# Performance work log

Hardware: AMD Instinct MI355X
Metric: run time of the kernel (lower is better)

## Reference

```python
import jax, jax.numpy as jnp
import numpy as np

B, N = 8, 32768
S1, S2, K = 512, 128, 32


def _knn_idx(refs, queries, k):
    # refs: (B,S,D), queries: (B,Q,D) -> (B,Q,k) indices of k nearest refs
    d = (jnp.sum(queries * queries, -1)[:, :, None]
         - 2.0 * jnp.einsum('bqd,bsd->bqs', queries, refs)
         + jnp.sum(refs * refs, -1)[:, None, :])
    _, idx = jax.lax.top_k(-d, k)
    return idx


def _gather(feats, idx):
    # feats: (B,S,C), idx: (B,Q,k) -> (B,Q,k,C)
    return jax.vmap(lambda f, i: f[i])(feats, idx)


def _mlp(x, w1, b1, w2, b2):
    # pointwise (1x1 conv) MLP: Linear -> ReLU -> Linear
    return jnp.maximum(x @ w1 + b1, 0.0) @ w2 + b2


def _set_abstraction(coords, feats, samp_idx, k, w1, b1, w2, b2):
    centers = coords[:, samp_idx]                 # (B,S,D)
    nidx = _knn_idx(coords, centers, k)           # (B,S,k)
    groups = _gather(feats, nidx)                 # (B,S,k,C)
    h = _mlp(groups, w1, b1, w2, b2)              # (B,S,k,C_out)
    return jnp.max(h, axis=2), centers


def _feature_prop(coords_q, feats_q, coords_s, feats_s, w1, b1, w2, b2):
    nidx = _knn_idx(coords_s, coords_q, 3)        # (B,Q,3)
    interp = jnp.mean(_gather(feats_s, nidx), axis=2)  # 3-NN average (sum/3)
    return _mlp(jnp.concatenate([feats_q, interp], -1), w1, b1, w2, b2)


def setup_inputs():
    key = jax.random.key(0)
    ks = jax.random.split(key, 12)

    def w(k, shape):
        return jax.random.normal(k, shape, jnp.float32) * 0.05

    z = lambda c: jnp.zeros((c,), jnp.float32)
    return {
        'x': jax.random.normal(ks[0], (B, N, 3), jnp.float32),
        'sa1_w1': w(ks[1], (3, 64)),   'sa1_b1': z(64),
        'sa1_w2': w(ks[2], (64, 64)),  'sa1_b2': z(64),
        'sa2_w1': w(ks[3], (64, 128)), 'sa2_b1': z(128),
        'sa2_w2': w(ks[4], (128, 128)),'sa2_b2': z(128),
        'fp1_w1': w(ks[5], (192, 64)), 'fp1_b1': z(64),
        'fp1_w2': w(ks[6], (64, 64)),  'fp1_b2': z(64),
        'fp2_w1': w(ks[7], (67, 32)),  'fp2_b1': z(32),
        'fp2_w2': w(ks[8], (32, 32)),  'fp2_b2': z(32),
        'fc_w': w(ks[9], (32, 2)),     'fc_b': z(2),
    }


def reference(x, sa1_w1, sa1_b1, sa1_w2, sa1_b2,
              sa2_w1, sa2_b1, sa2_w2, sa2_b2,
              fp1_w1, fp1_b1, fp1_w2, fp1_b2,
              fp2_w1, fp2_b1, fp2_w2, fp2_b2,
              fc_w, fc_b):
    rng = np.random.default_rng(0)
    samp1 = jnp.asarray(rng.permutation(N)[:S1])   # torch.randperm analog (static)
    samp2 = jnp.asarray(rng.permutation(S1)[:S2])

    f1, s1 = _set_abstraction(x, x, samp1, K, sa1_w1, sa1_b1, sa1_w2, sa1_b2)
    f2, s2 = _set_abstraction(s1, f1, samp2, K, sa2_w1, sa2_b1, sa2_w2, sa2_b2)
    g1 = _feature_prop(s1, f1, s2, f2, fp1_w1, fp1_b1, fp1_w2, fp1_b2)   # (B,512,64)
    g2 = _feature_prop(x, x, s1, g1, fp2_w1, fp2_b1, fp2_w2, fp2_b2)     # (B,N,32)
    logits = g2 @ fc_w + fc_b                                            # (B,N,2)
    return jax.nn.log_softmax(logits, axis=-1)
```

## Files before the change

### kernel.cpp

```cpp
#include <hip/hip_runtime.h>
#include <stdint.h>

#define B_ 8
#define N_ 32768
#define S1_ 512
#define S2_ 128

#define OFF_XR4   ((size_t)0)
#define OFF_C1    ((size_t)4194304)
#define OFF_C1R4  ((size_t)4243456)
#define OFF_C2    ((size_t)4308992)
#define OFF_NIDX1 ((size_t)4321280)
#define OFF_F1    ((size_t)4845568)
#define OFF_NIDX2 ((size_t)5369856)
#define OFF_F2    ((size_t)5500928)
#define OFF_G1    ((size_t)6025216)

struct Samps { int s1[S1_]; int s2[S2_]; };

typedef unsigned __int128 u128;
struct RngState { u128 state, inc; bool has32; uint32_t saved; };

static uint64_t rng_next64(RngState* r) {
  const u128 MULT = ((u128)0x2360ed051fc65da4ULL << 64) | 0x4385df649fccf645ULL;
  r->state = r->state * MULT + r->inc;
  uint64_t hi = (uint64_t)(r->state >> 64), lo = (uint64_t)r->state;
  uint64_t xs = hi ^ lo;
  unsigned rot = (unsigned)(r->state >> 122);
  return (xs >> rot) | (xs << ((64u - rot) & 63u));
}
static uint32_t rng_next32(RngState* r) {
  if (r->has32) { r->has32 = false; return r->saved; }
  uint64_t v = rng_next64(r);
  r->has32 = true; r->saved = (uint32_t)(v >> 32);
  return (uint32_t)v;
}
static uint32_t rng_interval(RngState* r, uint32_t mx) {
  if (mx == 0) return 0;
  uint32_t mask = mx;
  mask |= mask >> 1; mask |= mask >> 2; mask |= mask >> 4;
  mask |= mask >> 8; mask |= mask >> 16;
  uint32_t v;
  while ((v = (rng_next32(r) & mask)) > mx) {}
  return v;
}
static void compute_samples(int* s1, int* s2) {
  uint32_t pool[4];
  uint32_t hc = 0x43b0d7e5u;
  auto hmix = [&hc](uint32_t v) -> uint32_t {
    v ^= hc; hc *= 0x931e8875u; v *= hc; v ^= v >> 16; return v;
  };
  auto mixf = [](uint32_t x, uint32_t y) -> uint32_t {
    uint32_t rr = (x * 0xca01f9ddu) ^ (y * 0x4973f715u);
    rr ^= rr >> 16; return rr;
  };
  pool[0] = hmix(0u); pool[1] = hmix(0u); pool[2] = hmix(0u); pool[3] = hmix(0u);
  for (int s = 0; s < 4; ++s)
    for (int d = 0; d < 4; ++d)
      if (s != d) pool[d] = mixf(pool[d], hmix(pool[s]));
  uint32_t hc2 = 0x8b51f9ddu;
  uint32_t w32[8];
  for (int i = 0; i < 8; ++i) {
    uint32_t dv = pool[i & 3];
    dv ^= hc2; hc2 *= 0x58f38dedu; dv *= hc2; dv ^= dv >> 16;
    w32[i] = dv;
  }
  uint64_t w64[4];
  for (int i = 0; i < 4; ++i) w64[i] = (uint64_t)w32[2*i] | ((uint64_t)w32[2*i+1] << 32);
  const u128 MULT = ((u128)0x2360ed051fc65da4ULL << 64) | 0x4385df649fccf645ULL;
  u128 initstate = ((u128)w64[0] << 64) | w64[1];
  u128 initseq   = ((u128)w64[2] << 64) | w64[3];
  RngState r; r.has32 = false; r.saved = 0;
  r.inc = (initseq << 1) | 1;
  r.state = 0;
  r.state = r.state * MULT + r.inc;
  r.state += initstate;
  r.state = r.state * MULT + r.inc;
  static int perm1[N_];
  for (int i = 0; i < N_; ++i) perm1[i] = i;
  for (int i = N_ - 1; i > 0; --i) {
    uint32_t j = rng_interval(&r, (uint32_t)i);
    int t = perm1[i]; perm1[i] = perm1[j]; perm1[j] = t;
  }
  for (int i = 0; i < S1_; ++i) s1[i] = perm1[i];
  int perm2[S1_];
  for (int i = 0; i < S1_; ++i) perm2[i] = i;
  for (int i = S1_ - 1; i > 0; --i) {
    uint32_t j = rng_interval(&r, (uint32_t)i);
    int t = perm2[i]; perm2[i] = perm2[j]; perm2[j] = t;
  }
  for (int i = 0; i < S2_; ++i) s2[i] = perm2[i];
}


__global__ void k_prep(const float* __restrict__ x, float4* __restrict__ xr4) {
  int t = blockIdx.x * blockDim.x + threadIdx.x;
  float a = x[3*t], b = x[3*t+1], c = x[3*t+2];
  xr4[t] = make_float4(a, b, c, a*a + b*b + c*c);
}

__global__ void k_centers(const float* __restrict__ x, Samps sm,
                          float* __restrict__ c1, float4* __restrict__ c1r4,
                          float* __restrict__ c2) {
  int t = blockIdx.x * blockDim.x + threadIdx.x;
  if (t < B_*S1_) {
    int b = t >> 9, c = t & (S1_-1);
    int sidx = sm.s1[c];
    const float* src = x + ((size_t)b*N_ + sidx)*3;
    float a = src[0], bb = src[1], cc = src[2];
    c1[(size_t)t*3+0] = a; c1[(size_t)t*3+1] = bb; c1[(size_t)t*3+2] = cc;
    c1r4[t] = make_float4(a, bb, cc, a*a + bb*bb + cc*cc);
  } else {
    int u = t - B_*S1_;
    if (u < B_*S2_) {
      int b = u >> 7, c = u & (S2_-1);
      int sidx = sm.s1[sm.s2[c]];
      const float* src = x + ((size_t)b*N_ + sidx)*3;
      c2[(size_t)u*3+0] = src[0]; c2[(size_t)u*3+1] = src[1]; c2[(size_t)u*3+2] = src[2];
    }
  }
}

#define KNN_KEY(RV, UB)                                                     \
  {                                                                         \
    float dot = qx*(RV).x + qy*(RV).y + qz*(RV).z;                          \
    float dd = (qq - 2.0f*dot) + (RV).w;                                    \
    (UB) = __float_as_uint(dd);                                             \
    (UB) ^= ((unsigned int)((int)(UB) >> 31)) | 0x80000000u;                \
  }

#define KNN_INSERT(UB, PBASE)                                               \
  {                                                                         \
    bool cand = ((UB) < T);                                                 \
    while (__any(cand)) {                                                   \
      unsigned long long bal = __ballot(cand);                              \
      int src = (int)__builtin_ctzll(bal);                                  \
      unsigned int ikd = (unsigned int)__shfl((int)(UB), src);              \
      unsigned int iki = (unsigned int)((PBASE) + src);                     \
      int pos = __popcll(__ballot(ld <= ikd));                              \
      unsigned int ud = (unsigned int)__shfl_up((int)ld, 1);                \
      unsigned int ui = (unsigned int)__shfl_up((int)li, 1);                \
      if (lane == pos)      { ld = ikd; li = iki; }                         \
      else if (lane > pos)  { ld = ud;  li = ui;  }                         \
      T = (unsigned int)__shfl((int)ld, 31);                                \
      cand = cand && ((UB) < T) && (lane != src);                           \
    }                                                                       \
  }

__launch_bounds__(256)
__global__ void k_knn(const float4* __restrict__ refs4, const float* __restrict__ qpts,
                      int* __restrict__ out_idx, int nrefs, int qshift) {
  const int tid = threadIdx.x, lane = tid & 63;
  const int q = blockIdx.x * 4 + (tid >> 6);
  const int b = q >> qshift;
  const float4* refs = refs4 + (size_t)b * nrefs;
  float qx = qpts[(size_t)q*3+0], qy = qpts[(size_t)q*3+1], qz = qpts[(size_t)q*3+2];
  float qq = qx*qx + qy*qy + qz*qz;
  unsigned int ld, li, T;
  {
    float4 rv = refs[lane];
    unsigned int ub; KNN_KEY(rv, ub);
    unsigned long long key = ((unsigned long long)ub << 32) | (unsigned int)lane;
    #pragma unroll
    for (int k2 = 2; k2 <= 64; k2 <<= 1) {
      #pragma unroll
      for (int j = k2 >> 1; j >= 1; j >>= 1) {
        unsigned long long o = __shfl_xor(key, j);
        bool keepmin = (((lane & j) == 0) == ((lane & k2) == 0));
        if ((o < key) == keepmin) key = o;
      }
    }
    ld = (unsigned int)(key >> 32);
    li = (unsigned int)key;
    T = (unsigned int)__shfl((int)ld, 31);
  }
  {
    float4 r1 = refs[64 + lane];
    float4 r2 = refs[128 + lane];
    float4 r3 = refs[192 + lane];
    unsigned int u1, u2, u3;
    KNN_KEY(r1, u1); KNN_KEY(r2, u2); KNN_KEY(r3, u3);
    KNN_INSERT(u1, 64);
    KNN_INSERT(u2, 128);
    KNN_INSERT(u3, 192);
  }
  for (int g = 256; g + 255 < nrefs; g += 256) {
    float4 r0 = refs[g + lane];
    float4 r1 = refs[g + 64 + lane];
    float4 r2 = refs[g + 128 + lane];
    float4 r3 = refs[g + 192 + lane];
    unsigned int u0, u1, u2, u3;
    KNN_KEY(r0, u0); KNN_KEY(r1, u1); KNN_KEY(r2, u2); KNN_KEY(r3, u3);
    KNN_INSERT(u0, g);
    KNN_INSERT(u1, g + 64);
    KNN_INSERT(u2, g + 128);
    KNN_INSERT(u3, g + 192);
  }
  if (lane < 32) out_idx[(size_t)q*32 + lane] = (int)li;
}

__launch_bounds__(256)
__global__ void k_sa1mlp(const float* __restrict__ x, const int* __restrict__ nidx1,
                         const float* __restrict__ w1, const float* __restrict__ b1,
                         const float* __restrict__ w2, const float* __restrict__ b2,
                         float* __restrict__ f1) {
  __shared__ __align__(16) float hbuf[4][64];
  const int tid = threadIdx.x, wave = tid >> 6, lane = tid & 63;
  const int q = blockIdx.x * 4 + wave;
  const int b = q >> 9;
  const float* xb = x + (size_t)b * N_ * 3;
  float wc0 = w1[lane], wc1 = w1[64 + lane], wc2 = w1[128 + lane];
  float b1v = b1[lane], b2v = b2[lane];
  float w2c[64];
  #pragma unroll
  for (int h = 0; h < 64; ++h) w2c[h] = w2[h*64 + lane];
  const int* nb = nidx1 + (size_t)q * 32;
  int n0 = nb[0];
  float px = xb[3*n0], py = xb[3*n0+1], pz = xb[3*n0+2];
  float fm = -3.402823466e+38f;
  for (int j = 0; j < 32; ++j) {
    int n2 = nb[(j + 1) & 31];
    float nx = xb[3*n2], ny = xb[3*n2+1], nz = xb[3*n2+2];
    float h1 = fmaf(px, wc0, fmaf(py, wc1, fmaf(pz, wc2, b1v)));
    h1 = fmaxf(h1, 0.0f);
    hbuf[wave][lane] = h1;
    float acc = b2v;
    const float4* hv = (const float4*)(&hbuf[wave][0]);
    #pragma unroll
    for (int h4 = 0; h4 < 16; ++h4) {
      float4 v = hv[h4];
      acc = fmaf(v.x, w2c[4*h4+0], acc);
      acc = fmaf(v.y, w2c[4*h4+1], acc);
      acc = fmaf(v.z, w2c[4*h4+2], acc);
      acc = fmaf(v.w, w2c[4*h4+3], acc);
    }
    fm = fmaxf(fm, acc);
    px = nx; py = ny; pz = nz;
  }
  f1[(size_t)q*64 + lane] = fm;
}

__launch_bounds__(256)
__global__ void k_sa2mlp(const float* __restrict__ f1, const int* __restrict__ nidx2,
                         const float* __restrict__ w1, const float* __restrict__ b1,
                         const float* __restrict__ w2, const float* __restrict__ b2,
                         float* __restrict__ f2) {
  __shared__ __align__(16) float fin[64];
  __shared__ __align__(16) float h1s[128];
  __shared__ float ph[128];
  const int tid = threadIdx.x;
  const int s = tid >> 7, t = tid & 127;
  const int q = blockIdx.x;
  const int b = q >> 7;
  float w1r[32], w2r[64];
  #pragma unroll
  for (int i = 0; i < 32; ++i) w1r[i] = w1[(s*32 + i)*128 + t];
  #pragma unroll
  for (int h = 0; h < 64; ++h) w2r[h] = w2[(s*64 + h)*128 + t];
  float b1v = b1[t], b2v = b2[t];
  const int* nb = nidx2 + (size_t)q * 32;
  float fm = -3.402823466e+38f;
  for (int j = 0; j < 32; ++j) {
    int n = nb[j];
    __syncthreads();
    if (tid < 64) fin[tid] = f1[((size_t)b * S1_ + n)*64 + tid];
    __syncthreads();
    float p1 = 0.0f;
    const float4* fv = (const float4*)(fin + s*32);
    #pragma unroll
    for (int i4 = 0; i4 < 8; ++i4) {
      float4 v = fv[i4];
      p1 = fmaf(v.x, w1r[4*i4+0], p1);
      p1 = fmaf(v.y, w1r[4*i4+1], p1);
      p1 = fmaf(v.z, w1r[4*i4+2], p1);
      p1 = fmaf(v.w, w1r[4*i4+3], p1);
    }
    if (s) ph[t] = p1;
    __syncthreads();
    if (!s) h1s[t] = fmaxf(p1 + ph[t] + b1v, 0.0f);
    __syncthreads();
    float p2 = 0.0f;
    const float4* hv = (const float4*)(h1s + s*64);
    #pragma unroll
    for (int h4 = 0; h4 < 16; ++h4) {
      float4 v = hv[h4];
      p2 = fmaf(v.x, w2r[4*h4+0], p2);
      p2 = fmaf(v.y, w2r[4*h4+1], p2);
      p2 = fmaf(v.z, w2r[4*h4+2], p2);
      p2 = fmaf(v.w, w2r[4*h4+3], p2);
    }
    if (s) ph[t] = p2;
    __syncthreads();
    if (!s) fm = fmaxf(fm, p2 + ph[t] + b2v);
  }
  if (!s) f2[(size_t)q*128 + t] = fm;
}

__launch_bounds__(256)
__global__ void k_fp1(const float* __restrict__ c1, const float* __restrict__ c2,
                      const float* __restrict__ f1, const float* __restrict__ f2,
                      const float* __restrict__ w1, const float* __restrict__ b1,
                      const float* __restrict__ w2, const float* __restrict__ b2,
                      float* __restrict__ g1) {
  __shared__ __align__(16) float sw1[192*64];
  __shared__ __align__(16) float sw2[64*64];
  __shared__ __align__(16) float sinp[4][192];
  __shared__ __align__(16) float sh1[4][64];
  __shared__ __align__(16) float4 srefs4[S2_];
  const int tid = threadIdx.x;
  const int wave = tid >> 6, lane = tid & 63;
  const int q = blockIdx.x * 4 + wave;
  const int b = q >> 9;
  for (int i = tid; i < 192*64; i += 256) sw1[i] = w1[i];
  for (int i = tid; i < 64*64; i += 256) sw2[i] = w2[i];
  if (tid < S2_) {
    const float* rp = c2 + ((size_t)b * S2_ + tid) * 3;
    float rx = rp[0], ry = rp[1], rz = rp[2];
    srefs4[tid] = make_float4(rx, ry, rz, rx*rx + ry*ry + rz*rz);
  }
  __syncthreads();
  float qx = c1[(size_t)q*3+0], qy = c1[(size_t)q*3+1], qz = c1[(size_t)q*3+2];
  float qq = qx*qx + qy*qy + qz*qz;
  unsigned long long ka, kb;
  {
    float4 rv = srefs4[lane];
    float dot = qx*rv.x + qy*rv.y + qz*rv.z;
    float d = (qq - 2.0f*dot) + rv.w;
    unsigned int ub = __float_as_uint(d);
    ub ^= ((unsigned int)((int)ub >> 31)) | 0x80000000u;
    ka = ((unsigned long long)ub << 32) | (unsigned int)lane;
    rv = srefs4[lane + 64];
    dot = qx*rv.x + qy*rv.y + qz*rv.z;
    d = (qq - 2.0f*dot) + rv.w;
    ub = __float_as_uint(d);
    ub ^= ((unsigned int)((int)ub >> 31)) | 0x80000000u;
    kb = ((unsigned long long)ub << 32) | (unsigned int)(lane + 64);
    if (kb < ka) { unsigned long long tt = ka; ka = kb; kb = tt; }
  }
  int nsel[3];
  #pragma unroll
  for (int r = 0; r < 3; ++r) {
    unsigned long long m = ka;
    #pragma unroll
    for (int s = 1; s < 64; s <<= 1) {
      unsigned long long o = __shfl_xor(m, s);
      if (o < m) m = o;
    }
    nsel[r] = (int)(m & 0xffffffffu);
    if (ka == m) { ka = kb; kb = ~0ULL; }
  }
  const float* f2b = f2 + (size_t)b * S2_ * 128;
  sinp[wave][lane] = f1[(size_t)q*64 + lane];
  {
    float a0 = f2b[(size_t)nsel[0]*128 + lane];
    float a1 = f2b[(size_t)nsel[1]*128 + lane];
    float a2 = f2b[(size_t)nsel[2]*128 + lane];
    sinp[wave][64 + lane] = (a0 + a1 + a2) / 3.0f;
    a0 = f2b[(size_t)nsel[0]*128 + 64 + lane];
    a1 = f2b[(size_t)nsel[1]*128 + 64 + lane];
    a2 = f2b[(size_t)nsel[2]*128 + 64 + lane];
    sinp[wave][128 + lane] = (a0 + a1 + a2) / 3.0f;
  }
  __syncthreads();
  float acc = b1[lane];
  const float4* sv = (const float4*)(&sinp[wave][0]);
  #pragma unroll
  for (int i4 = 0; i4 < 48; ++i4) {
    float4 v = sv[i4];
    acc = fmaf(v.x, sw1[(4*i4+0)*64 + lane], acc);
    acc = fmaf(v.y, sw1[(4*i4+1)*64 + lane], acc);
    acc = fmaf(v.z, sw1[(4*i4+2)*64 + lane], acc);
    acc = fmaf(v.w, sw1[(4*i4+3)*64 + lane], acc);
  }
  sh1[wave][lane] = fmaxf(acc, 0.0f);
  __syncthreads();
  float acc2 = b2[lane];
  const float4* hv = (const float4*)(&sh1[wave][0]);
  #pragma unroll
  for (int h4 = 0; h4 < 16; ++h4) {
    float4 v = hv[h4];
    acc2 = fmaf(v.x, sw2[(4*h4+0)*64 + lane], acc2);
    acc2 = fmaf(v.y, sw2[(4*h4+1)*64 + lane], acc2);
    acc2 = fmaf(v.z, sw2[(4*h4+2)*64 + lane], acc2);
    acc2 = fmaf(v.w, sw2[(4*h4+3)*64 + lane], acc2);
  }
  g1[(size_t)q*64 + lane] = acc2;
}

#define FP2_PROC(RV, R)                                                     \
  {                                                                         \
    float dot = qx*(RV).x + qy*(RV).y + qz*(RV).z;                          \
    float dd = (qq - 2.0f*dot) + (RV).w;                                    \
    bool c0 = dd < d0, c1 = dd < d1, c2 = dd < d2;                          \
    i2 = c1 ? i1 : (c2 ? (R) : i2);                                         \
    d2 = c1 ? d1 : fminf(d2, dd);                                           \
    i1 = c0 ? i0 : (c1 ? (R) : i1);                                         \
    d1 = c0 ? d0 : fminf(d1, dd);                                           \
    i0 = c0 ? (R) : i0;                                                     \
    d0 = fminf(d0, dd);                                                     \
  }

__launch_bounds__(256)
__global__ void k_fp2(const float* __restrict__ x, const float4* __restrict__ c1r4,
                      const float* __restrict__ g1,
                      const float* __restrict__ w1, const float* __restrict__ b1,
                      const float* __restrict__ w2, const float* __restrict__ b2,
                      const float* __restrict__ fcw, const float* __restrict__ fcb,
                      float* __restrict__ out) {
  __shared__ __align__(16) float sw1[67*32];
  __shared__ __align__(16) float sw2[32*32];
  __shared__ __align__(16) float sfc[64];
  __shared__ float sb1[32], sb2[32], sfcb[2];
  const int tid = threadIdx.x;
  const int b = blockIdx.x >> 7;
  const int n = ((blockIdx.x & 127) << 8) + tid;
  for (int i = tid; i < 67*32; i += 256) sw1[i] = w1[i];
  for (int i = tid; i < 32*32; i += 256) sw2[i] = w2[i];
  if (tid < 64) sfc[tid] = fcw[tid];
  if (tid < 32) { sb1[tid] = b1[tid]; sb2[tid] = b2[tid]; }
  if (tid < 2) sfcb[tid] = fcb[tid];
  __syncthreads();
  const float* xb = x + (size_t)b * N_ * 3;
  float qx = xb[3*n], qy = xb[3*n+1], qz = xb[3*n+2];
  float qq = qx*qx + qy*qy + qz*qz;
  const float4* refs = c1r4 + (size_t)b * S1_;
  float d0 = 3.402823466e+38f, d1 = d0, d2 = d0;
  int i0 = 0, i1 = 0, i2 = 0;
  for (int r = 0; r < S1_; r += 4) {
    float4 ra = refs[r+0];
    float4 rb = refs[r+1];
    float4 rc = refs[r+2];
    float4 rd = refs[r+3];
    FP2_PROC(ra, r+0);
    FP2_PROC(rb, r+1);
    FP2_PROC(rc, r+2);
    FP2_PROC(rd, r+3);
  }
  const float* g1b = g1 + (size_t)b * S1_ * 64;
  const float4* p0 = (const float4*)(g1b + (size_t)i0 * 64);
  const float4* p1 = (const float4*)(g1b + (size_t)i1 * 64);
  const float4* p2 = (const float4*)(g1b + (size_t)i2 * 64);
  const float THIRD = 1.0f / 3.0f;
  float h1r[32];
  #pragma unroll
  for (int k = 0; k < 32; ++k) h1r[k] = sb1[k];
  #pragma unroll
  for (int i = 0; i < 3; ++i) {
    float v = (i == 0) ? qx : (i == 1) ? qy : qz;
    const float4* wrow = (const float4*)(sw1 + i*32);
    #pragma unroll
    for (int kq = 0; kq < 8; ++kq) {
      float4 wv = wrow[kq];
      h1r[4*kq+0] = fmaf(v, wv.x, h1r[4*kq+0]);
      h1r[4*kq+1] = fmaf(v, wv.y, h1r[4*kq+1]);
      h1r[4*kq+2] = fmaf(v, wv.z, h1r[4*kq+2]);
      h1r[4*kq+3] = fmaf(v, wv.w, h1r[4*kq+3]);
    }
  }
  #pragma unroll 4
  for (int o = 0; o < 16; ++o) {
    float4 a = p0[o], bq = p1[o], cq = p2[o];
    float vv[4];
    vv[0] = (a.x + bq.x + cq.x) * THIRD;
    vv[1] = (a.y + bq.y + cq.y) * THIRD;
    vv[2] = (a.z + bq.z + cq.z) * THIRD;
    vv[3] = (a.w + bq.w + cq.w) * THIRD;
    #pragma unroll
    for (int j = 0; j < 4; ++j) {
      float v = vv[j];
      const float4* wrow = (const float4*)(sw1 + (3 + 4*o + j)*32);
      #pragma unroll
      for (int kq = 0; kq < 8; ++kq) {
        float4 wv = wrow[kq];
        h1r[4*kq+0] = fmaf(v, wv.x, h1r[4*kq+0]);
        h1r[4*kq+1] = fmaf(v, wv.y, h1r[4*kq+1]);
        h1r[4*kq+2] = fmaf(v, wv.z, h1r[4*kq+2]);
        h1r[4*kq+3] = fmaf(v, wv.w, h1r[4*kq+3]);
      }
    }
  }
  #pragma unroll
  for (int k = 0; k < 32; ++k) h1r[k] = fmaxf(h1r[k], 0.0f);
  float h2r[32];
  #pragma unroll
  for (int m = 0; m < 32; ++m) h2r[m] = sb2[m];
  #pragma unroll
  for (int k = 0; k < 32; ++k) {
    float v = h1r[k];
    const float4* wrow = (const float4*)(sw2 + k*32);
    #pragma unroll
    for (int mq = 0; mq < 8; ++mq) {
      float4 wv = wrow[mq];
      h2r[4*mq+0] = fmaf(v, wv.x, h2r[4*mq+0]);
      h2r[4*mq+1] = fmaf(v, wv.y, h2r[4*mq+1]);
      h2r[4*mq+2] = fmaf(v, wv.z, h2r[4*mq+2]);
      h2r[4*mq+3] = fmaf(v, wv.w, h2r[4*mq+3]);
    }
  }
  float l0 = sfcb[0], l1 = sfcb[1];
  #pragma unroll
  for (int m = 0; m < 32; ++m) {
    l0 = fmaf(h2r[m], sfc[2*m+0], l0);
    l1 = fmaf(h2r[m], sfc[2*m+1], l1);
  }
  float mx = fmaxf(l0, l1);
  float s0 = l0 - mx, s1 = l1 - mx;
  float lg = logf(expf(s0) + expf(s1));
  float2 res; res.x = s0 - lg; res.y = s1 - lg;
  ((float2*)out)[(size_t)b * N_ + n] = res;
}

extern "C" void kernel_launch(void* const* d_in, const int* in_sizes, int n_in,
                              void* d_out, int out_size, void* d_ws, size_t ws_size,
                              hipStream_t stream) {
  (void)in_sizes; (void)n_in; (void)out_size; (void)ws_size;
  const float* x     = (const float*)d_in[0];
  const float* sa1w1 = (const float*)d_in[1];
  const float* sa1b1 = (const float*)d_in[2];
  const float* sa1w2 = (const float*)d_in[3];
  const float* sa1b2 = (const float*)d_in[4];
  const float* sa2w1 = (const float*)d_in[5];
  const float* sa2b1 = (const float*)d_in[6];
  const float* sa2w2 = (const float*)d_in[7];
  const float* sa2b2 = (const float*)d_in[8];
  const float* fp1w1 = (const float*)d_in[9];
  const float* fp1b1 = (const float*)d_in[10];
  const float* fp1w2 = (const float*)d_in[11];
  const float* fp1b2 = (const float*)d_in[12];
  const float* fp2w1 = (const float*)d_in[13];
  const float* fp2b1 = (const float*)d_in[14];
  const float* fp2w2 = (const float*)d_in[15];
  const float* fp2b2 = (const float*)d_in[16];
  const float* fcw   = (const float*)d_in[17];
  const float* fcb   = (const float*)d_in[18];
  float* out = (float*)d_out;
  char* ws = (char*)d_ws;
  float4* xr4  = (float4*)(ws + OFF_XR4);
  float*  c1   = (float*)(ws + OFF_C1);
  float4* c1r4 = (float4*)(ws + OFF_C1R4);
  float*  c2   = (float*)(ws + OFF_C2);
  int*    nidx1= (int*)(ws + OFF_NIDX1);
  float*  f1   = (float*)(ws + OFF_F1);
  int*    nidx2= (int*)(ws + OFF_NIDX2);
  float*  f2   = (float*)(ws + OFF_F2);
  float*  g1   = (float*)(ws + OFF_G1);

  Samps smp;
  compute_samples(smp.s1, smp.s2);

  hipLaunchKernelGGL(k_prep,    dim3(B_*N_/256), dim3(256), 0, stream, x, xr4);
  hipLaunchKernelGGL(k_centers, dim3((B_*(S1_+S2_)+255)/256), dim3(256), 0, stream,
                     x, smp, c1, c1r4, c2);
  hipLaunchKernelGGL(k_knn,     dim3(B_*S1_/4), dim3(256), 0, stream, xr4, c1, nidx1, N_, 9);
  hipLaunchKernelGGL(k_sa1mlp,  dim3(B_*S1_/4), dim3(256), 0, stream,
                     x, nidx1, sa1w1, sa1b1, sa1w2, sa1b2, f1);
  hipLaunchKernelGGL(k_knn,     dim3(B_*S2_/4), dim3(256), 0, stream, c1r4, c2, nidx2, S1_, 7);
  hipLaunchKernelGGL(k_sa2mlp,  dim3(B_*S2_), dim3(256), 0, stream,
                     f1, nidx2, sa2w1, sa2b1, sa2w2, sa2b2, f2);
  hipLaunchKernelGGL(k_fp1,     dim3(B_*S1_/4), dim3(256), 0, stream,
                     c1, c2, f1, f2, fp1w1, fp1b1, fp1w2, fp1b2, g1);
  hipLaunchKernelGGL(k_fp2,     dim3(B_*N_/256), dim3(256), 0, stream,
                     x, c1r4, g1, fp2w1, fp2b1, fp2w2, fp2b2, fcw, fcb, out);
}
```

Baseline: 403.0 us.

## Split KNN reference scan across two waves per query and merge top-32

The KNN kernel now assigns two wavefronts to each query, each scanning half of the reference points and keeping its own sorted top-32 list. The two lists are merged through shared memory with a bitonic merge step. The insertion loop also switches from order-preserving uint keys to raw float compares, dropping the per-candidate key encoding. This doubles the number of waves available to hide latency on the long serial scan of 32768 points, at the cost of a block sync and a merge. Tie handling changes from < to <=, which may alter which index is chosen among equal distances.

```diff
diff --git a/kernel.cpp b/kernel.cpp
--- a/kernel.cpp
+++ b/kernel.cpp
@@ -129,38 +129,48 @@
     (UB) ^= ((unsigned int)((int)(UB) >> 31)) | 0x80000000u;                \
   }
 
-#define KNN_INSERT(UB, PBASE)                                               \
+#define KNN_DIST(RV, DD)                                                    \
   {                                                                         \
-    bool cand = ((UB) < T);                                                 \
+    float dot = qx*(RV).x + qy*(RV).y + qz*(RV).z;                          \
+    (DD) = (qq - 2.0f*dot) + (RV).w;                                        \
+  }
+
+#define KNN_INS_F(DD, PBASE)                                                \
+  {                                                                         \
+    bool cand = ((DD) <= Tf);                                               \
     while (__any(cand)) {                                                   \
       unsigned long long bal = __ballot(cand);                              \
       int src = (int)__builtin_ctzll(bal);                                  \
-      unsigned int ikd = (unsigned int)__shfl((int)(UB), src);              \
-      unsigned int iki = (unsigned int)((PBASE) + src);                     \
-      int pos = __popcll(__ballot(ld <= ikd));                              \
-      unsigned int ud = (unsigned int)__shfl_up((int)ld, 1);                \
-      unsigned int ui = (unsigned int)__shfl_up((int)li, 1);                \
-      if (lane == pos)      { ld = ikd; li = iki; }                         \
-      else if (lane > pos)  { ld = ud;  li = ui;  }                         \
-      T = (unsigned int)__shfl((int)ld, 31);                                \
-      cand = cand && ((UB) < T) && (lane != src);                           \
+      float df = __shfl((DD), src);                                         \
+      int ii = (PBASE) + src;                                               \
+      int pos = __popcll(__ballot(ldf <= df));                              \
+      float ud = __shfl_up(ldf, 1);                                         \
+      int ui = __shfl_up(li, 1);                                            \
+      if (lane == pos)      { ldf = df; li = ii; }                          \
+      else if (lane > pos)  { ldf = ud; li = ui;  }                         \
+      Tf = __shfl(ldf, 31);                                                 \
+      cand = cand && ((DD) <= Tf) && (lane != src);                         \
     }                                                                       \
   }
 
-__launch_bounds__(256)
-__global__ void k_knn(const float4* __restrict__ refs4, const float* __restrict__ qpts,
-                      int* __restrict__ out_idx, int nrefs, int qshift) {
-  const int tid = threadIdx.x, lane = tid & 63;
-  const int q = blockIdx.x * 4 + (tid >> 6);
+__launch_bounds__(128)
+__global__ void k_knn2(const float4* __restrict__ refs4, const float* __restrict__ qpts,
+                       int* __restrict__ out_idx, int nrefs, int qshift) {
+  __shared__ unsigned long long kbuf[64];
+  const int tid = threadIdx.x, lane = tid & 63, wv = tid >> 6;
+  const int q = blockIdx.x;
   const int b = q >> qshift;
   const float4* refs = refs4 + (size_t)b * nrefs;
+  const int half = nrefs >> 1;
+  const int base = wv * half;
   float qx = qpts[(size_t)q*3+0], qy = qpts[(size_t)q*3+1], qz = qpts[(size_t)q*3+2];
   float qq = qx*qx + qy*qy + qz*qz;
-  unsigned int ld, li, T;
+  float ldf, Tf;
+  int li;
   {
-    float4 rv = refs[lane];
+    float4 rv = refs[base + lane];
     unsigned int ub; KNN_KEY(rv, ub);
-    unsigned long long key = ((unsigned long long)ub << 32) | (unsigned int)lane;
+    unsigned long long key = ((unsigned long long)ub << 32) | (unsigned int)(base + lane);
     #pragma unroll
     for (int k2 = 2; k2 <= 64; k2 <<= 1) {
       #pragma unroll
@@ -170,33 +180,53 @@
         if ((o < key) == keepmin) key = o;
       }
     }
-    ld = (unsigned int)(key >> 32);
-    li = (unsigned int)key;
-    T = (unsigned int)__shfl((int)ld, 31);
+    unsigned int td = (unsigned int)(key >> 32);
+    li = (int)(key & 0xffffffffu);
+    int tt = (int)td >> 31;
+    unsigned int mask = tt ? 0x80000000u : 0xFFFFFFFFu;
+    ldf = __uint_as_float(td ^ mask);
+    Tf = __shfl(ldf, 31);
   }
   {
-    float4 r1 = refs[64 + lane];
-    float4 r2 = refs[128 + lane];
-    float4 r3 = refs[192 + lane];
-    unsigned int u1, u2, u3;
-    KNN_KEY(r1, u1); KNN_KEY(r2, u2); KNN_KEY(r3, u3);
-    KNN_INSERT(u1, 64);
-    KNN_INSERT(u2, 128);
-    KNN_INSERT(u3, 192);
-  }
-  for (int g = 256; g + 255 < nrefs; g += 256) {
+    float4 r1 = refs[base + 64 + lane];
+    float4 r2 = refs[base + 128 + lane];
+    float4 r3 = refs[base + 192 + lane];
+    float dd1, dd2, dd3;
+    KNN_DIST(r1, dd1); KNN_DIST(r2, dd2); KNN_DIST(r3, dd3);
+    KNN_INS_F(dd1, base + 64);
+    KNN_INS_F(dd2, base + 128);
+    KNN_INS_F(dd3, base + 192);
+  }
+  for (int g = base + 256; g + 255 < base + half; g += 256) {
     float4 r0 = refs[g + lane];
     float4 r1 = refs[g + 64 + lane];
     float4 r2 = refs[g + 128 + lane];
     float4 r3 = refs[g + 192 + lane];
-    unsigned int u0, u1, u2, u3;
-    KNN_KEY(r0, u0); KNN_KEY(r1, u1); KNN_KEY(r2, u2); KNN_KEY(r3, u3);
-    KNN_INSERT(u0, g);
-    KNN_INSERT(u1, g + 64);
-    KNN_INSERT(u2, g + 128);
-    KNN_INSERT(u3, g + 192);
-  }
-  if (lane < 32) out_idx[(size_t)q*32 + lane] = (int)li;
+    float dd0, dd1, dd2, dd3;
+    KNN_DIST(r0, dd0); KNN_DIST(r1, dd1); KNN_DIST(r2, dd2); KNN_DIST(r3, dd3);
+    KNN_INS_F(dd0, g);
+    KNN_INS_F(dd1, g + 64);
+    KNN_INS_F(dd2, g + 128);
+    KNN_INS_F(dd3, g + 192);
+  }
+  {
+    unsigned int ub2 = __float_as_uint(ldf);
+    ub2 ^= ((unsigned int)((int)ub2 >> 31)) | 0x80000000u;
+    unsigned long long key = ((unsigned long long)ub2 << 32) | (unsigned int)li;
+    if (lane < 32) kbuf[wv * 32 + lane] = key;
+  }
+  __syncthreads();
+  if (wv == 0) {
+    int srcl = (lane < 32) ? lane : (95 - lane);
+    unsigned long long v = kbuf[srcl];
+    #pragma unroll
+    for (int j = 32; j >= 1; j >>= 1) {
+      unsigned long long o = __shfl_xor(v, j);
+      bool keepmin = ((lane & j) == 0);
+      if ((o < v) == keepmin) v = o;
+    }
+    if (lane < 32) out_idx[(size_t)q*32 + lane] = (int)(v & 0xffffffffu);
+  }
 }
 
 __launch_bounds__(256)
@@ -551,10 +581,10 @@
   hipLaunchKernelGGL(k_prep,    dim3(B_*N_/256), dim3(256), 0, stream, x, xr4);
   hipLaunchKernelGGL(k_centers, dim3((B_*(S1_+S2_)+255)/256), dim3(256), 0, stream,
                      x, smp, c1, c1r4, c2);
-  hipLaunchKernelGGL(k_knn,     dim3(B_*S1_/4), dim3(256), 0, stream, xr4, c1, nidx1, N_, 9);
+  hipLaunchKernelGGL(k_knn2,    dim3(B_*S1_), dim3(128), 0, stream, xr4, c1, nidx1, N_, 9);
   hipLaunchKernelGGL(k_sa1mlp,  dim3(B_*S1_/4), dim3(256), 0, stream,
                      x, nidx1, sa1w1, sa1b1, sa1w2, sa1b2, f1);
-  hipLaunchKernelGGL(k_knn,     dim3(B_*S2_/4), dim3(256), 0, stream, c1r4, c2, nidx2, S1_, 7);
+  hipLaunchKernelGGL(k_knn2,    dim3(B_*S2_), dim3(128), 0, stream, c1r4, c2, nidx2, S1_, 7);
   hipLaunchKernelGGL(k_sa2mlp,  dim3(B_*S2_), dim3(256), 0, stream,
                      f1, nidx2, sa2w1, sa2b1, sa2w2, sa2b2, f2);
   hipLaunchKernelGGL(k_fp1,     dim3(B_*S1_/4), dim3(256), 0, stream,
```

New measurement: 397.7 us. No clear change (-1.3%).
